# Kernel tuning notes

Measured on AMD Instinct MI355X. Metric: run time of the kernel, lower is better.

Reference implementation:

```python
import jax, jax.numpy as jnp
import numpy as np
from jax import lax

B, C, H, W = 32, 256, 56, 56
NH, LC, DIL = 8, 7, 8  # heads, window size, dilation; H == LC*DIL -> exact dilated partition
N = LC * LC
DH = C // NH
SCALE = DH ** (-0.5)


def _rel_index():
    ch = np.arange(LC)
    coords = np.stack(np.meshgrid(ch, ch, indexing='ij')).reshape(2, -1)  # (2, 49)
    rel = (coords[:, :, None] - coords[:, None, :]).transpose(1, 2, 0)  # (49,49,2)
    rel[..., 0] += LC - 1
    rel[..., 1] += LC - 1
    rel[..., 0] *= 2 * LC - 1
    return jnp.asarray(rel.sum(-1))  # (49,49) int

REL_IDX = _rel_index()


def _layernorm(x, w, b, eps=1e-5):
    m = x.mean(-1, keepdims=True)
    v = ((x - m) ** 2).mean(-1, keepdims=True)
    return (x - m) * lax.rsqrt(v + eps) * w + b


def setup_inputs() -> dict:
    key = jax.random.key(0)
    ks = jax.random.split(key, 8)
    def n(k, shape, s=0.02):
        return jax.random.normal(k, shape, jnp.float32) * s
    return {
        'x': jax.random.normal(ks[0], (B, C, H, W), jnp.float32),
        'cpe_w': n(ks[1], (C, 1, 3, 3)),
        'cpe_b': jnp.zeros((C,), jnp.float32),
        'ln1_w': jnp.ones((C,), jnp.float32),
        'ln1_b': jnp.zeros((C,), jnp.float32),
        'rpb': n(ks[2], ((2 * LC - 1) ** 2, NH)),
        'qkv_w': n(ks[3], (C, 3 * C)),
        'qkv_b': jnp.zeros((3 * C,), jnp.float32),
        'proj_w': n(ks[4], (C, C)),
        'proj_b': jnp.zeros((C,), jnp.float32),
        'ln2_w': jnp.ones((C,), jnp.float32),
        'ln2_b': jnp.zeros((C,), jnp.float32),
        'fc1_w': n(ks[5], (C, 4 * C)),
        'fc1_b': jnp.zeros((4 * C,), jnp.float32),
        'fc2_w': n(ks[6], (4 * C, C)),
        'fc2_b': jnp.zeros((C,), jnp.float32),
    }


def reference(x, cpe_w, cpe_b, ln1_w, ln1_b, rpb, qkv_w, qkv_b, proj_w, proj_b,
              ln2_w, ln2_b, fc1_w, fc1_b, fc2_w, fc2_b):
    # CPE: depthwise 3x3 conv, residual
    cpe = lax.conv_general_dilated(x, cpe_w, (1, 1), 'SAME',
                                   dimension_numbers=('NCHW', 'OIHW', 'NCHW'),
                                   feature_group_count=C)
    x = x + cpe + cpe_b[None, :, None, None]
    x = x.transpose(0, 2, 3, 1)  # B,H,W,C
    shortcut = x
    xn = _layernorm(x, ln1_w, ln1_b)
    # dilated window partition (LD!=0): window (i,j) gathers pixels (i+DIL*t, j+DIL*u)
    xw = xn.reshape(B, LC, DIL, LC, DIL, C).transpose(0, 2, 4, 1, 3, 5)  # B,i,j,t,u,C
    x1 = xw.reshape(B * DIL * DIL, N, C)
    # window attention with relative position bias
    qkv = (x1 @ qkv_w + qkv_b).reshape(-1, N, 3, NH, DH).transpose(2, 0, 3, 1, 4)
    q, k, v = qkv[0] * SCALE, qkv[1], qkv[2]  # (Bn,NH,N,DH)
    attn = jnp.einsum('bhnd,bhmd->bhnm', q, k)
    bias = rpb[REL_IDX].transpose(2, 0, 1)  # (NH,N,N)
    attn = jax.nn.softmax(attn + bias[None], axis=-1)
    o = jnp.einsum('bhnm,bhmd->bhnd', attn, v).transpose(0, 2, 1, 3).reshape(-1, N, C)
    o = o @ proj_w + proj_b
    # scatter windows back to spatial positions (exact inverse of the partition)
    o = o.reshape(B, DIL, DIL, LC, LC, C).transpose(0, 3, 1, 4, 2, 5).reshape(B, H, W, C)
    x = shortcut + o
    h = _layernorm(x, ln2_w, ln2_b)
    h = jax.nn.gelu(h @ fc1_w + fc1_b, approximate=False) @ fc2_w + fc2_b
    x = x + h
    return x.transpose(0, 3, 1, 2)  # B,C,H,W
```

## Files before the change

kernel.cpp:

```cpp
#include <hip/hip_runtime.h>
#include <hip/hip_bf16.h>

#define DEVINL __device__ __forceinline__

constexpr int Cc  = 256;
constexpr int Hh  = 56;
constexpr int Ww  = 56;
constexpr int Tn  = 32 * 56 * 56;
constexpr int HW  = Hh * Ww;
constexpr float SCALEF = 0.17677669529663689f;

typedef __attribute__((ext_vector_type(4))) float f32x4;
typedef __attribute__((ext_vector_type(8))) short bf16x8;

DEVINL unsigned short f2bf(float f) {
  __hip_bfloat16 h = __float2bfloat16(f);
  return *reinterpret_cast<unsigned short*>(&h);
}
DEVINL float bf2f(unsigned short u) {
  union { unsigned int i; float f; } v; v.i = (unsigned int)u << 16; return v.f;
}

#define GLOAD_LDS16(gp, lp) \
  __builtin_amdgcn_global_load_lds((const __attribute__((address_space(1))) void*)(gp), \
                                   (__attribute__((address_space(3))) void*)(lp), 16, 0, 0)

__global__ __launch_bounds__(256) void cpe_kernel(const float* __restrict__ x,
    const float* __restrict__ cw, const float* __restrict__ cb,
    unsigned short* __restrict__ out)
{
  __shared__ unsigned short Xs[16 * 581];
  const int tid = threadIdx.x;
  const int bx  = blockIdx.x;
  const int cg  = bx & 15;
  const int t2  = bx >> 4;
  const int hg  = t2 % 7;
  const int b   = t2 / 7;
  const int c0  = cg * 16;
  const int h0  = hg * 8;

  for (int idx = tid; idx < 16 * 580; idx += 256) {
    const int ci  = idx / 580;
    const int rem = idx - ci * 580;
    const int rr  = rem / 58;
    const int wc  = rem - rr * 58;
    const int h2  = h0 - 1 + rr;
    const int w2  = wc - 1;
    float v = 0.f;
    if (h2 >= 0 && h2 < Hh && w2 >= 0 && w2 < Ww)
      v = x[((size_t)(b * Cc + c0 + ci)) * HW + h2 * Ww + w2];
    Xs[ci * 581 + rem] = f2bf(v);
  }
  __syncthreads();

  const int ci = tid & 15;
  const int c  = c0 + ci;
  float wr9[9];
  #pragma unroll
  for (int i = 0; i < 9; ++i) wr9[i] = cw[c * 9 + i];
  const float cbv = cb[c];
  const unsigned short* Xc = Xs + ci * 581;

  #pragma unroll
  for (int it = 0; it < 7; ++it) {
    const int tg   = it * 16 + (tid >> 4);
    const int tok0 = tg * 4;
    const int hr   = tok0 / 56;
    const int w0   = tok0 - hr * 56;
    float r0v[6], r1v[6], r2v[6];
    #pragma unroll
    for (int j = 0; j < 6; ++j) {
      r0v[j] = bf2f(Xc[hr * 58 + w0 + j]);
      r1v[j] = bf2f(Xc[(hr + 1) * 58 + w0 + j]);
      r2v[j] = bf2f(Xc[(hr + 2) * 58 + w0 + j]);
    }
    unsigned short ov[4];
    #pragma unroll
    for (int t = 0; t < 4; ++t) {
      float acc = r1v[t + 1];
      acc += wr9[0] * r0v[t] + wr9[1] * r0v[t + 1] + wr9[2] * r0v[t + 2];
      acc += wr9[3] * r1v[t] + wr9[4] * r1v[t + 1] + wr9[5] * r1v[t + 2];
      acc += wr9[6] * r2v[t] + wr9[7] * r2v[t + 1] + wr9[8] * r2v[t + 2];
      ov[t] = f2bf(acc + cbv);
    }
    const size_t tbase = (size_t)b * HW + (h0 + hr) * Ww + w0;
    #pragma unroll
    for (int t = 0; t < 4; ++t)
      out[(tbase + t) * Cc + c] = ov[t];
  }
}

__global__ __launch_bounds__(256) void stats_bf16(const unsigned short* __restrict__ in,
    float2* __restrict__ st)
{
  const int lane = threadIdx.x & 63;
  const size_t t = (size_t)blockIdx.x * 4 + (threadIdx.x >> 6);
  const ushort4 v = *reinterpret_cast<const ushort4*>(in + t * Cc + lane * 4);
  const float v0 = bf2f(v.x), v1 = bf2f(v.y), v2 = bf2f(v.z), v3 = bf2f(v.w);
  float s  = v0 + v1 + v2 + v3;
  float sq = v0 * v0 + v1 * v1 + v2 * v2 + v3 * v3;
  #pragma unroll
  for (int o = 32; o >= 1; o >>= 1) {
    s  += __shfl_xor(s, o);
    sq += __shfl_xor(sq, o);
  }
  if (lane == 0) {
    const float mean = s * (1.0f / Cc);
    const float var  = sq * (1.0f / Cc) - mean * mean;
    st[t] = make_float2(mean, rsqrtf(var + 1e-5f));
  }
}

__global__ __launch_bounds__(256) void ln_apply_bf16(const unsigned short* __restrict__ inp,
    const float* __restrict__ w, const float* __restrict__ b,
    unsigned short* __restrict__ out)
{
  const int lane = threadIdx.x & 63;
  const size_t t = (size_t)blockIdx.x * 4 + (threadIdx.x >> 6);
  const ushort4 v = *reinterpret_cast<const ushort4*>(inp + t * Cc + lane * 4);
  const float v0 = bf2f(v.x), v1 = bf2f(v.y), v2 = bf2f(v.z), v3 = bf2f(v.w);
  float s  = v0 + v1 + v2 + v3;
  float sq = v0 * v0 + v1 * v1 + v2 * v2 + v3 * v3;
  #pragma unroll
  for (int o = 32; o >= 1; o >>= 1) {
    s  += __shfl_xor(s, o);
    sq += __shfl_xor(sq, o);
  }
  const float mean = s * (1.0f / Cc);
  const float var  = sq * (1.0f / Cc) - mean * mean;
  const float r    = rsqrtf(var + 1e-5f);
  const float4 w4 = *reinterpret_cast<const float4*>(w + lane * 4);
  const float4 b4 = *reinterpret_cast<const float4*>(b + lane * 4);
  ushort4 o;
  o.x = f2bf((v0 - mean) * r * w4.x + b4.x);
  o.y = f2bf((v1 - mean) * r * w4.y + b4.y);
  o.z = f2bf((v2 - mean) * r * w4.z + b4.z);
  o.w = f2bf((v3 - mean) * r * w4.w + b4.w);
  *reinterpret_cast<ushort4*>(out + t * Cc + lane * 4) = o;
}

template<int QS>
__global__ __launch_bounds__(256) void wconv_kernel(const float* __restrict__ W,
    const float* __restrict__ g, unsigned short* __restrict__ Wt, int K, int N)
{
  __shared__ float Xs[32][33];
  const int kb = blockIdx.x * 32, nb = blockIdx.y * 32;
  const int tn = threadIdx.x & 31, tk = threadIdx.x >> 5;
  #pragma unroll
  for (int i = 0; i < 4; ++i) {
    const int k = kb + tk + i * 8;
    const float gv = g ? g[k] : 1.0f;
    Xs[tk + i * 8][tn] = W[(size_t)k * N + nb + tn] * gv;
  }
  __syncthreads();
  const int wk = threadIdx.x & 31, wn = threadIdx.x >> 5;
  #pragma unroll
  for (int i = 0; i < 4; ++i) {
    const int n = nb + wn + i * 8;
    const float s = (QS && n < 256) ? SCALEF : 1.0f;
    Wt[(size_t)n * K + kb + wk] = f2bf(Xs[wk][wn + i * 8] * s);
  }
}

template<int S>
__global__ __launch_bounds__(256) void colsum_kernel(const float* __restrict__ W,
    const float* __restrict__ g, const float* __restrict__ bvec,
    const float* __restrict__ bias, float* __restrict__ C1, float* __restrict__ CB,
    int K, int N)
{
  __shared__ float red[2][256];
  const int col = blockIdx.x * 64 + (threadIdx.x & 63);
  const int ks  = threadIdx.x >> 6;
  const int kq  = K >> 2;
  float a1 = 0.f, a2 = 0.f;
  for (int k = ks * kq; k < (ks + 1) * kq; ++k) {
    const float wv = W[(size_t)k * N + col];
    a1 += g[k] * wv;
    a2 += bvec[k] * wv;
  }
  red[0][threadIdx.x] = a1;
  red[1][threadIdx.x] = a2;
  __syncthreads();
  if (threadIdx.x < 64) {
    float s1 = 0.f, s2 = 0.f;
    #pragma unroll
    for (int i = 0; i < 4; ++i) { s1 += red[0][threadIdx.x + i * 64]; s2 += red[1][threadIdx.x + i * 64]; }
    const float sc = (S && col < 256) ? SCALEF : 1.0f;
    C1[col] = sc * s1;
    CB[col] = sc * (s2 + bias[col]);
  }
}

__global__ __launch_bounds__(256) void biasgen_kernel(const float* __restrict__ rpb,
    float* __restrict__ biasT)
{
  const int i = blockIdx.x * 256 + threadIdx.x;
  const int h = i >> 12, n = (i >> 6) & 63, m = i & 63;
  float v;
  if (m >= 49) {
    v = -1e30f;
  } else {
    const int nc = n < 49 ? n : 48;
    const int dI = nc / 7 - m / 7 + 6;
    const int dJ = nc % 7 - m % 7 + 6;
    v = rpb[(dI * 13 + dJ) * 8 + h];
  }
  biasT[i] = v;
}

template<int EPI, int OSW>
__global__ __launch_bounds__(256) void mfma_gemm(
    const unsigned short* __restrict__ A, const unsigned short* __restrict__ Bt,
    const float* __restrict__ bias, const float* __restrict__ C1,
    const float2* __restrict__ stats, const unsigned short* __restrict__ resp,
    void* __restrict__ outp, int K, int N, int row0, int n_outer, int n_inner)
{
  __shared__ unsigned short Asm[128 * 64];
  __shared__ unsigned short Bsm[128 * 64];
  const int tid  = threadIdx.x;
  const int lane = tid & 63;
  const int wid  = tid >> 6;
  const int wr   = wid >> 1;
  const int wc   = wid & 1;

  int outer, inner;
  if ((n_outer & 7) == 0) {
    const int slot = blockIdx.x >> 3;
    outer = (slot / n_inner) * 8 + (blockIdx.x & 7);
    inner = slot - (slot / n_inner) * n_inner;
  } else {
    outer = blockIdx.x / n_inner;
    inner = blockIdx.x - outer * n_inner;
  }
  const int bm = (OSW ? inner : outer) * 128;
  const int bn = (OSW ? outer : inner) * 128;

  f32x4 acc[4][4] = {};

  const int srow = (lane >> 3);
  const int skc  = ((lane & 7) ^ srow) * 8;

  for (int k0 = 0; k0 < K; k0 += 64) {
    #pragma unroll
    for (int i = 0; i < 4; ++i) {
      const int ch  = wid * 4 + i;
      const int row = ch * 8 + srow;
      GLOAD_LDS16(A  + (size_t)(bm + row) * K + k0 + skc, &Asm[ch * 512]);
      GLOAD_LDS16(Bt + (size_t)(bn + row) * K + k0 + skc, &Bsm[ch * 512]);
    }
    __syncthreads();

    const int xr = lane & 7;
    const int lg = lane >> 4;
    #pragma unroll
    for (int k32 = 0; k32 < 2; ++k32) {
      const int koff = ((k32 * 4 + lg) ^ xr) * 8;
      bf16x8 af[4], bv[4];
      #pragma unroll
      for (int f = 0; f < 4; ++f) {
        af[f] = *reinterpret_cast<const bf16x8*>(
            &Asm[(wr * 64 + f * 16 + (lane & 15)) * 64 + koff]);
        bv[f] = *reinterpret_cast<const bf16x8*>(
            &Bsm[(wc * 64 + f * 16 + (lane & 15)) * 64 + koff]);
      }
      #pragma unroll
      for (int fm = 0; fm < 4; ++fm)
        #pragma unroll
        for (int fn = 0; fn < 4; ++fn)
          acc[fm][fn] = __builtin_amdgcn_mfma_f32_16x16x32_bf16(
              af[fm], bv[fn], acc[fm][fn], 0, 0, 0);
    }
    __syncthreads();
  }

  const int lr4 = (lane >> 4) * 4;
  const int lc  = lane & 15;
  if constexpr (EPI == 0) {
    float rsv[4][4], rmv[4][4];
    #pragma unroll
    for (int fm = 0; fm < 4; ++fm)
      #pragma unroll
      for (int r = 0; r < 4; ++r) {
        const float2 st = stats[bm + wr * 64 + fm * 16 + lr4 + r];
        rsv[fm][r] = st.y;
        rmv[fm][r] = -st.y * st.x;
      }
    #pragma unroll
    for (int fn = 0; fn < 4; ++fn) {
      const int gcol = bn + wc * 64 + fn * 16 + lc;
      const float c1 = C1[gcol], cb = bias[gcol];
      #pragma unroll
      for (int fm = 0; fm < 4; ++fm)
        #pragma unroll
        for (int r = 0; r < 4; ++r) {
          const int grow = bm + wr * 64 + fm * 16 + lr4 + r;
          const float v = rsv[fm][r] * acc[fm][fn][r] + rmv[fm][r] * c1 + cb;
          ((unsigned short*)outp)[(size_t)grow * N + gcol] = f2bf(v);
        }
    }
  } else if constexpr (EPI == 4) {
    float bch[4][4];
    #pragma unroll
    for (int fm = 0; fm < 4; ++fm)
      #pragma unroll
      for (int r = 0; r < 4; ++r)
        bch[fm][r] = bias[bm + wr * 64 + fm * 16 + lr4 + r];
    #pragma unroll
    for (int fn = 0; fn < 4; ++fn) {
      const int gtok = bn + wc * 64 + fn * 16 + lc;
      const int mg = row0 + gtok;
      const int b  = mg / HW;
      const int sp = mg - b * HW;
      float* ob = (float*)outp + (size_t)b * 256 * HW + sp;
      #pragma unroll
      for (int fm = 0; fm < 4; ++fm)
        #pragma unroll
        for (int r = 0; r < 4; ++r) {
          const int ch = bm + wr * 64 + fm * 16 + lr4 + r;
          float v = acc[fm][fn][r] + bch[fm][r];
          v += bf2f(resp[(size_t)gtok * 256 + ch]);
          ob[(size_t)ch * HW] = v;
        }
    }
  } else {
    #pragma unroll
    for (int fn = 0; fn < 4; ++fn) {
      const int gcol = bn + wc * 64 + fn * 16 + lc;
      const float bvs = bias[gcol];
      #pragma unroll
      for (int fm = 0; fm < 4; ++fm) {
        #pragma unroll
        for (int r = 0; r < 4; ++r) {
          const int grow = bm + wr * 64 + fm * 16 + lr4 + r;
          float v = acc[fm][fn][r] + bvs;
          if constexpr (EPI == 1) {
            v += bf2f(resp[(size_t)grow * 256 + gcol]);
            ((unsigned short*)outp)[(size_t)grow * N + gcol] = f2bf(v);
          } else {
            const float z = 1.5957691f * (v + 0.044715f * v * v * v);
            v = v / (1.0f + __expf(-z));
            ((unsigned short*)outp)[(size_t)grow * N + gcol] = f2bf(v);
          }
        }
      }
    }
  }
}

__global__ __launch_bounds__(256) void attn_mfma(const unsigned short* __restrict__ qkv,
    const float* __restrict__ biasT, unsigned short* __restrict__ outD)
{
  __shared__ char smem[4 * 14848];
  const int tid  = threadIdx.x;
  const int lane = tid & 63;
  const int wid  = tid >> 6;
  char* base = smem + wid * 14848;
  char* Qs = base;
  char* Ks = base + 5120;
  char* Vt = base + 10240;
  char* Ps = base;

  const int blk = blockIdx.x;
  const int b   = blk >> 6;
  const int di  = (blk >> 3) & 7;
  const int dj  = blk & 7;
  const size_t t00 = (size_t)b * HW + di * Ww + dj;

  const int lg = lane >> 4;
  const int lc = lane & 15;

  for (int rep = 0; rep < 2; ++rep) {
    const int h = wid * 2 + rep;

    for (int i = lane; i < 300; i += 64) {
      if (i < 150) reinterpret_cast<unsigned long long*>(Qs + 49 * 80)[i] = 0ull;
      else         reinterpret_cast<unsigned long long*>(Ks + 49 * 80)[i - 150] = 0ull;
    }
    for (int i = lane; i < 192; i += 64) {
      const int row = i / 6, q = i - (i / 6) * 6;
      *reinterpret_cast<unsigned long long*>(Vt + row * 144 + 96 + q * 8) = 0ull;
    }

    for (int idx = lane; idx < 392; idx += 64) {
      const int row = idx >> 3, dq = idx & 7;
      const int li = row / 7, lj = row - (row / 7) * 7;
      const size_t t = t00 + (size_t)(li * 8) * Ww + lj * 8;
      const unsigned short* src = qkv + t * 768 + h * 32 + dq * 4;
      *reinterpret_cast<uint2*>(Qs + row * 80 + dq * 8) =
          *reinterpret_cast<const uint2*>(src);
      *reinterpret_cast<uint2*>(Ks + row * 80 + dq * 8) =
          *reinterpret_cast<const uint2*>(src + 256);
    }
    for (int idx = lane; idx < 784; idx += 64) {
      const int row = idx >> 4, q = idx & 15;
      const int li = row / 7, lj = row - (row / 7) * 7;
      const size_t t = t00 + (size_t)(li * 8) * Ww + lj * 8;
      const unsigned int v = *reinterpret_cast<const unsigned int*>(
          qkv + t * 768 + h * 32 + 512 + q * 2);
      *reinterpret_cast<unsigned short*>(Vt + (2 * q) * 144 + row * 2) =
          (unsigned short)(v & 0xffff);
      *reinterpret_cast<unsigned short*>(Vt + (2 * q + 1) * 144 + row * 2) =
          (unsigned short)(v >> 16);
    }

    f32x4 sacc[4][4] = {};
    {
      bf16x8 af[4], bv[4];
      #pragma unroll
      for (int f = 0; f < 4; ++f) {
        af[f] = *reinterpret_cast<const bf16x8*>(Qs + (f * 16 + lc) * 80 + lg * 16);
        bv[f] = *reinterpret_cast<const bf16x8*>(Ks + (f * 16 + lc) * 80 + lg * 16);
      }
      #pragma unroll
      for (int fm = 0; fm < 4; ++fm)
        #pragma unroll
        for (int fn = 0; fn < 4; ++fn)
          sacc[fm][fn] = __builtin_amdgcn_mfma_f32_16x16x32_bf16(
              af[fm], bv[fn], sacc[fm][fn], 0, 0, 0);
    }

    const float* bh = biasT + h * 4096;
    #pragma unroll
    for (int fm = 0; fm < 4; ++fm) {
      float rowv[4][4];
      #pragma unroll
      for (int r = 0; r < 4; ++r) {
        const int n = fm * 16 + lg * 4 + r;
        #pragma unroll
        for (int fn = 0; fn < 4; ++fn)
          rowv[r][fn] = sacc[fm][fn][r] + bh[n * 64 + fn * 16 + lc];
      }
      #pragma unroll
      for (int r = 0; r < 4; ++r) {
        float mx = fmaxf(fmaxf(rowv[r][0], rowv[r][1]), fmaxf(rowv[r][2], rowv[r][3]));
        #pragma unroll
        for (int o = 8; o >= 1; o >>= 1) mx = fmaxf(mx, __shfl_xor(mx, o));
        float p[4], sm = 0.f;
        #pragma unroll
        for (int fn = 0; fn < 4; ++fn) { p[fn] = __expf(rowv[r][fn] - mx); sm += p[fn]; }
        #pragma unroll
        for (int o = 8; o >= 1; o >>= 1) sm += __shfl_xor(sm, o);
        const float inv = 1.0f / sm;
        const int n = fm * 16 + lg * 4 + r;
        #pragma unroll
        for (int fn = 0; fn < 4; ++fn)
          *reinterpret_cast<unsigned short*>(Ps + n * 144 + (fn * 16 + lc) * 2) =
              f2bf(p[fn] * inv);
      }
    }

    f32x4 oacc[4][2] = {};
    #pragma unroll
    for (int ks = 0; ks < 2; ++ks) {
      bf16x8 pa[4], vb[2];
      #pragma unroll
      for (int fm = 0; fm < 4; ++fm)
        pa[fm] = *reinterpret_cast<const bf16x8*>(
            Ps + (fm * 16 + lc) * 144 + ks * 64 + lg * 16);
      #pragma unroll
      for (int fn = 0; fn < 2; ++fn)
        vb[fn] = *reinterpret_cast<const bf16x8*>(
            Vt + (fn * 16 + lc) * 144 + ks * 64 + lg * 16);
      #pragma unroll
      for (int fm = 0; fm < 4; ++fm)
        #pragma unroll
        for (int fn = 0; fn < 2; ++fn)
          oacc[fm][fn] = __builtin_amdgcn_mfma_f32_16x16x32_bf16(
              pa[fm], vb[fn], oacc[fm][fn], 0, 0, 0);
    }

    #pragma unroll
    for (int fm = 0; fm < 4; ++fm) {
      #pragma unroll
      for (int r = 0; r < 4; ++r) {
        const int n = fm * 16 + lg * 4 + r;
        if (n < 49) {
          const int li = n / 7, lj = n - (n / 7) * 7;
          const size_t t = t00 + (size_t)(li * 8) * Ww + lj * 8;
          outD[t * 256 + h * 32 + lc]      = f2bf(oacc[fm][0][r]);
          outD[t * 256 + h * 32 + 16 + lc] = f2bf(oacc[fm][1][r]);
        }
      }
    }
  }
}

extern "C" void kernel_launch(void* const* d_in, const int* in_sizes, int n_in,
                              void* d_out, int out_size, void* d_ws, size_t ws_size,
                              hipStream_t stream) {
  (void)in_sizes; (void)n_in; (void)out_size;
  const float* x      = (const float*)d_in[0];
  const float* cpe_w  = (const float*)d_in[1];
  const float* cpe_b  = (const float*)d_in[2];
  const float* ln1_w  = (const float*)d_in[3];
  const float* ln1_b  = (const float*)d_in[4];
  const float* rpb    = (const float*)d_in[5];
  const float* qkv_w  = (const float*)d_in[6];
  const float* qkv_b  = (const float*)d_in[7];
  const float* proj_w = (const float*)d_in[8];
  const float* proj_b = (const float*)d_in[9];
  const float* ln2_w  = (const float*)d_in[10];
  const float* ln2_b  = (const float*)d_in[11];
  const float* fc1_w  = (const float*)d_in[12];
  const float* fc1_b  = (const float*)d_in[13];
  const float* fc2_w  = (const float*)d_in[14];
  const float* fc2_b  = (const float*)d_in[15];

  char* ws = (char*)d_ws;
  unsigned short* qkv_wt  = (unsigned short*)(ws);
  unsigned short* proj_wt = (unsigned short*)(ws + 393216);
  unsigned short* fc1_wt  = (unsigned short*)(ws + 524288);
  unsigned short* fc2_wt  = (unsigned short*)(ws + 1048576);
  float*  C1q = (float*)(ws + 1572864);
  float*  CBq = (float*)(ws + 1575936);

  int NB_rt;
  if      (ws_size >= 311000000ull) NB_rt = 32;
  else if (ws_size >= 157000000ull) NB_rt = 16;
  else                              NB_rt = 8;
  const int MCHrt = NB_rt * HW;
  const int NCH   = 32 / NB_rt;
  const int NOUT  = MCHrt / 128;

  unsigned short *slotX, *slotQ, *slotE;
  float2* statsFull = nullptr;
  float*  biasTp;
  if (NB_rt == 8) {
    slotX  = (unsigned short*)(ws + 1579008);
    slotQ  = (unsigned short*)(ws + 14424064);
    slotE  = (unsigned short*)(ws + 65804288);
    biasTp = (float*)(ws + 65804288 + 200704);
  } else {
    biasTp    = (float*)(ws + 1579008);
    statsFull = (float2*)(ws + 1710080);
    size_t o = 2512896;
    slotX = (unsigned short*)(ws + o); o += (size_t)MCHrt * 256 * 2;
    slotQ = (unsigned short*)(ws + o); o += (size_t)MCHrt * 1024 * 2;
    slotE = (unsigned short*)(ws + o);
  }

  unsigned short* Araw = (unsigned short*)d_out + 25690112;

  wconv_kernel<1><<<dim3(8, 24), 256, 0, stream>>>(qkv_w,  ln1_w,  qkv_wt,  256, 768);
  wconv_kernel<0><<<dim3(8, 8),  256, 0, stream>>>(proj_w, nullptr, proj_wt, 256, 256);
  wconv_kernel<0><<<dim3(8, 32), 256, 0, stream>>>(fc1_w,  nullptr, fc1_wt,  256, 1024);
  wconv_kernel<0><<<dim3(32, 8), 256, 0, stream>>>(fc2_w,  nullptr, fc2_wt,  1024, 256);
  colsum_kernel<1><<<12, 256, 0, stream>>>(qkv_w, ln1_w, ln1_b, qkv_b, C1q, CBq, 256, 768);

  cpe_kernel<<<32 * 7 * 16, 256, 0, stream>>>(x, cpe_w, cpe_b, Araw);

  if (NB_rt != 8) {
    stats_bf16<<<Tn / 4, 256, 0, stream>>>(Araw, statsFull);
    biasgen_kernel<<<128, 256, 0, stream>>>(rpb, biasTp);
  }

  for (int c = 0; c < NCH; ++c) {
    const int r0 = c * MCHrt;
    const unsigned short* Ac = Araw + (size_t)r0 * Cc;
    const float2* stp;
    if (NB_rt == 8) {
      float2* stloc = (float2*)slotE;
      stats_bf16<<<MCHrt / 4, 256, 0, stream>>>(Ac, stloc);
      biasgen_kernel<<<128, 256, 0, stream>>>(rpb, biasTp);
      stp = stloc;
    } else {
      stp = statsFull + r0;
    }
    mfma_gemm<0, 0><<<NOUT * 6, 256, 0, stream>>>(
        Ac, qkv_wt, CBq, C1q, stp, nullptr, slotQ, 256, 768, 0, NOUT, 6);
    attn_mfma<<<NB_rt * 64, 256, 0, stream>>>(slotQ, biasTp, slotX);
    mfma_gemm<1, 0><<<NOUT * 2, 256, 0, stream>>>(
        slotX, proj_wt, proj_b, nullptr, nullptr, Ac, slotE, 256, 256, 0, NOUT, 2);
    ln_apply_bf16<<<MCHrt / 4, 256, 0, stream>>>(slotE, ln2_w, ln2_b, slotX);
    mfma_gemm<2, 0><<<NOUT * 8, 256, 0, stream>>>(
        slotX, fc1_wt, fc1_b, nullptr, nullptr, nullptr, slotQ, 256, 1024, 0, NOUT, 8);
    mfma_gemm<4, 1><<<NOUT * 2, 256, 0, stream>>>(
        fc2_wt, slotQ, fc2_b, nullptr, nullptr, slotE, d_out, 1024, 256, r0, NOUT, 2);
  }
}
```

Before: 662.3 us.

## Cap token chunk at 16 images and split MLP into halves for L2 residency

```diff
diff --git a/kernel.cpp b/kernel.cpp
--- a/kernel.cpp
+++ b/kernel.cpp
@@ -223,15 +223,10 @@
   const int wr   = wid >> 1;
   const int wc   = wid & 1;
 
-  int outer, inner;
-  if ((n_outer & 7) == 0) {
-    const int slot = blockIdx.x >> 3;
-    outer = (slot / n_inner) * 8 + (blockIdx.x & 7);
-    inner = slot - (slot / n_inner) * n_inner;
-  } else {
-    outer = blockIdx.x / n_inner;
-    inner = blockIdx.x - outer * n_inner;
-  }
+  const int slot  = blockIdx.x >> 3;
+  const int outer = (slot / n_inner) * 8 + (blockIdx.x & 7);
+  const int inner = slot - (slot / n_inner) * n_inner;
+  if (outer >= n_outer) return;
   const int bm = (OSW ? inner : outer) * 128;
   const int bn = (OSW ? outer : inner) * 128;
 
@@ -514,10 +509,7 @@
   float*  C1q = (float*)(ws + 1572864);
   float*  CBq = (float*)(ws + 1575936);
 
-  int NB_rt;
-  if      (ws_size >= 311000000ull) NB_rt = 32;
-  else if (ws_size >= 157000000ull) NB_rt = 16;
-  else                              NB_rt = 8;
+  const int NB_rt = (ws_size >= 157000000ull) ? 16 : 8;
   const int MCHrt = NB_rt * HW;
   const int NCH   = 32 / NB_rt;
   const int NOUT  = MCHrt / 128;
@@ -535,7 +527,7 @@
     statsFull = (float2*)(ws + 1710080);
     size_t o = 2512896;
     slotX = (unsigned short*)(ws + o); o += (size_t)MCHrt * 256 * 2;
-    slotQ = (unsigned short*)(ws + o); o += (size_t)MCHrt * 1024 * 2;
+    slotQ = (unsigned short*)(ws + o); o += (size_t)MCHrt * 768 * 2;
     slotE = (unsigned short*)(ws + o);
   }
 
@@ -572,9 +564,25 @@
     mfma_gemm<1, 0><<<NOUT * 2, 256, 0, stream>>>(
         slotX, proj_wt, proj_b, nullptr, nullptr, Ac, slotE, 256, 256, 0, NOUT, 2);
     ln_apply_bf16<<<MCHrt / 4, 256, 0, stream>>>(slotE, ln2_w, ln2_b, slotX);
-    mfma_gemm<2, 0><<<NOUT * 8, 256, 0, stream>>>(
-        slotX, fc1_wt, fc1_b, nullptr, nullptr, nullptr, slotQ, 256, 1024, 0, NOUT, 8);
-    mfma_gemm<4, 1><<<NOUT * 2, 256, 0, stream>>>(
-        fc2_wt, slotQ, fc2_b, nullptr, nullptr, slotE, d_out, 1024, 256, r0, NOUT, 2);
-  }
-}
+
+    if (NB_rt == 8) {
+      mfma_gemm<2, 0><<<((NOUT + 7) & ~7) * 8, 256, 0, stream>>>(
+          slotX, fc1_wt, fc1_b, nullptr, nullptr, nullptr, slotQ, 256, 1024, 0, NOUT, 8);
+      mfma_gemm<4, 1><<<((NOUT + 7) & ~7) * 2, 256, 0, stream>>>(
+          fc2_wt, slotQ, fc2_b, nullptr, nullptr, slotE, d_out, 1024, 256, r0, NOUT, 2);
+    } else {
+      const int HTOK = MCHrt / 2;
+      const int NOH  = HTOK / 128;
+      const int NOHP = (NOH + 7) & ~7;
+      for (int half = 0; half < 2; ++half) {
+        const int off = half * HTOK;
+        mfma_gemm<2, 0><<<NOHP * 8, 256, 0, stream>>>(
+            slotX + (size_t)off * 256, fc1_wt, fc1_b, nullptr, nullptr, nullptr,
+            slotQ, 256, 1024, 0, NOH, 8);
+        mfma_gemm<4, 1><<<NOHP * 2, 256, 0, stream>>>(
+            fc2_wt, slotQ, fc2_b, nullptr, nullptr, slotE + (size_t)off * 256,
+            d_out, 1024, 256, r0 + off, NOH, 2);
+      }
+    }
+  }
+}
```

New measurement: 679.9 us. 2.7% more time.

## Fold LN2 into fc1 GEMM epilogue, pad CPE LDS rows, unify block swizzle

Applied to the files above, without the earlier changes.

```diff
diff --git a/kernel.cpp b/kernel.cpp
--- a/kernel.cpp
+++ b/kernel.cpp
@@ -20,6 +20,10 @@
 DEVINL float bf2f(unsigned short u) {
   union { unsigned int i; float f; } v; v.i = (unsigned int)u << 16; return v.f;
 }
+DEVINL float gelu_fast(float v) {
+  const float z = 1.5957691f * (v + 0.044715f * v * v * v);
+  return v / (1.0f + __expf(-z));
+}
 
 #define GLOAD_LDS16(gp, lp) \
   __builtin_amdgcn_global_load_lds((const __attribute__((address_space(1))) void*)(gp), \
@@ -29,7 +33,7 @@
     const float* __restrict__ cw, const float* __restrict__ cb,
     unsigned short* __restrict__ out)
 {
-  __shared__ unsigned short Xs[16 * 581];
+  __shared__ unsigned short Xs[16 * 620];
   const int tid = threadIdx.x;
   const int bx  = blockIdx.x;
   const int cg  = bx & 15;
@@ -49,7 +53,7 @@
     float v = 0.f;
     if (h2 >= 0 && h2 < Hh && w2 >= 0 && w2 < Ww)
       v = x[((size_t)(b * Cc + c0 + ci)) * HW + h2 * Ww + w2];
-    Xs[ci * 581 + rem] = f2bf(v);
+    Xs[ci * 620 + rr * 60 + wc] = f2bf(v);
   }
   __syncthreads();
 
@@ -59,7 +63,7 @@
   #pragma unroll
   for (int i = 0; i < 9; ++i) wr9[i] = cw[c * 9 + i];
   const float cbv = cb[c];
-  const unsigned short* Xc = Xs + ci * 581;
+  const unsigned short* Xc = Xs + ci * 620;
 
   #pragma unroll
   for (int it = 0; it < 7; ++it) {
@@ -67,20 +71,21 @@
     const int tok0 = tg * 4;
     const int hr   = tok0 / 56;
     const int w0   = tok0 - hr * 56;
-    float r0v[6], r1v[6], r2v[6];
-    #pragma unroll
-    for (int j = 0; j < 6; ++j) {
-      r0v[j] = bf2f(Xc[hr * 58 + w0 + j]);
-      r1v[j] = bf2f(Xc[(hr + 1) * 58 + w0 + j]);
-      r2v[j] = bf2f(Xc[(hr + 2) * 58 + w0 + j]);
+    float rv[3][6];
+    #pragma unroll
+    for (int j = 0; j < 3; ++j) {
+      const ushort4 a = *reinterpret_cast<const ushort4*>(Xc + (hr + j) * 60 + w0);
+      const ushort2 e = *reinterpret_cast<const ushort2*>(Xc + (hr + j) * 60 + w0 + 4);
+      rv[j][0] = bf2f(a.x); rv[j][1] = bf2f(a.y); rv[j][2] = bf2f(a.z);
+      rv[j][3] = bf2f(a.w); rv[j][4] = bf2f(e.x); rv[j][5] = bf2f(e.y);
     }
     unsigned short ov[4];
     #pragma unroll
     for (int t = 0; t < 4; ++t) {
-      float acc = r1v[t + 1];
-      acc += wr9[0] * r0v[t] + wr9[1] * r0v[t + 1] + wr9[2] * r0v[t + 2];
-      acc += wr9[3] * r1v[t] + wr9[4] * r1v[t + 1] + wr9[5] * r1v[t + 2];
-      acc += wr9[6] * r2v[t] + wr9[7] * r2v[t + 1] + wr9[8] * r2v[t + 2];
+      float acc = rv[1][t + 1];
+      acc += wr9[0] * rv[0][t] + wr9[1] * rv[0][t + 1] + wr9[2] * rv[0][t + 2];
+      acc += wr9[3] * rv[1][t] + wr9[4] * rv[1][t + 1] + wr9[5] * rv[1][t + 2];
+      acc += wr9[6] * rv[2][t] + wr9[7] * rv[2][t + 1] + wr9[8] * rv[2][t + 2];
       ov[t] = f2bf(acc + cbv);
     }
     const size_t tbase = (size_t)b * HW + (h0 + hr) * Ww + w0;
@@ -111,34 +116,6 @@
   }
 }
 
-__global__ __launch_bounds__(256) void ln_apply_bf16(const unsigned short* __restrict__ inp,
-    const float* __restrict__ w, const float* __restrict__ b,
-    unsigned short* __restrict__ out)
-{
-  const int lane = threadIdx.x & 63;
-  const size_t t = (size_t)blockIdx.x * 4 + (threadIdx.x >> 6);
-  const ushort4 v = *reinterpret_cast<const ushort4*>(inp + t * Cc + lane * 4);
-  const float v0 = bf2f(v.x), v1 = bf2f(v.y), v2 = bf2f(v.z), v3 = bf2f(v.w);
-  float s  = v0 + v1 + v2 + v3;
-  float sq = v0 * v0 + v1 * v1 + v2 * v2 + v3 * v3;
-  #pragma unroll
-  for (int o = 32; o >= 1; o >>= 1) {
-    s  += __shfl_xor(s, o);
-    sq += __shfl_xor(sq, o);
-  }
-  const float mean = s * (1.0f / Cc);
-  const float var  = sq * (1.0f / Cc) - mean * mean;
-  const float r    = rsqrtf(var + 1e-5f);
-  const float4 w4 = *reinterpret_cast<const float4*>(w + lane * 4);
-  const float4 b4 = *reinterpret_cast<const float4*>(b + lane * 4);
-  ushort4 o;
-  o.x = f2bf((v0 - mean) * r * w4.x + b4.x);
-  o.y = f2bf((v1 - mean) * r * w4.y + b4.y);
-  o.z = f2bf((v2 - mean) * r * w4.z + b4.z);
-  o.w = f2bf((v3 - mean) * r * w4.w + b4.w);
-  *reinterpret_cast<ushort4*>(out + t * Cc + lane * 4) = o;
-}
-
 template<int QS>
 __global__ __launch_bounds__(256) void wconv_kernel(const float* __restrict__ W,
     const float* __restrict__ g, unsigned short* __restrict__ Wt, int K, int N)
@@ -223,15 +200,10 @@
   const int wr   = wid >> 1;
   const int wc   = wid & 1;
 
-  int outer, inner;
-  if ((n_outer & 7) == 0) {
-    const int slot = blockIdx.x >> 3;
-    outer = (slot / n_inner) * 8 + (blockIdx.x & 7);
-    inner = slot - (slot / n_inner) * n_inner;
-  } else {
-    outer = blockIdx.x / n_inner;
-    inner = blockIdx.x - outer * n_inner;
-  }
+  const int slot  = blockIdx.x >> 3;
+  const int outer = (slot / n_inner) * 8 + (blockIdx.x & 7);
+  const int inner = slot - (slot / n_inner) * n_inner;
+  if (outer >= n_outer) return;
   const int bm = (OSW ? inner : outer) * 128;
   const int bn = (OSW ? outer : inner) * 128;
 
@@ -275,7 +247,7 @@
 
   const int lr4 = (lane >> 4) * 4;
   const int lc  = lane & 15;
-  if constexpr (EPI == 0) {
+  if constexpr (EPI == 0 || EPI == 5) {
     float rsv[4][4], rmv[4][4];
     #pragma unroll
     for (int fm = 0; fm < 4; ++fm)
@@ -294,7 +266,8 @@
         #pragma unroll
         for (int r = 0; r < 4; ++r) {
           const int grow = bm + wr * 64 + fm * 16 + lr4 + r;
-          const float v = rsv[fm][r] * acc[fm][fn][r] + rmv[fm][r] * c1 + cb;
+          float v = rsv[fm][r] * acc[fm][fn][r] + rmv[fm][r] * c1 + cb;
+          if constexpr (EPI == 5) v = gelu_fast(v);
           ((unsigned short*)outp)[(size_t)grow * N + gcol] = f2bf(v);
         }
     }
@@ -333,14 +306,8 @@
         for (int r = 0; r < 4; ++r) {
           const int grow = bm + wr * 64 + fm * 16 + lr4 + r;
           float v = acc[fm][fn][r] + bvs;
-          if constexpr (EPI == 1) {
-            v += bf2f(resp[(size_t)grow * 256 + gcol]);
-            ((unsigned short*)outp)[(size_t)grow * N + gcol] = f2bf(v);
-          } else {
-            const float z = 1.5957691f * (v + 0.044715f * v * v * v);
-            v = v / (1.0f + __expf(-z));
-            ((unsigned short*)outp)[(size_t)grow * N + gcol] = f2bf(v);
-          }
+          v += bf2f(resp[(size_t)grow * 256 + gcol]);
+          ((unsigned short*)outp)[(size_t)grow * N + gcol] = f2bf(v);
         }
       }
     }
@@ -513,27 +480,27 @@
   unsigned short* fc2_wt  = (unsigned short*)(ws + 1048576);
   float*  C1q = (float*)(ws + 1572864);
   float*  CBq = (float*)(ws + 1575936);
-
-  int NB_rt;
-  if      (ws_size >= 311000000ull) NB_rt = 32;
-  else if (ws_size >= 157000000ull) NB_rt = 16;
-  else                              NB_rt = 8;
+  float*  C1f = (float*)(ws + 1579008);
+  float*  CBf = (float*)(ws + 1583104);
+
+  const int NB_rt = (ws_size >= 311000000ull) ? 32 : 8;
   const int MCHrt = NB_rt * HW;
   const int NCH   = 32 / NB_rt;
   const int NOUT  = MCHrt / 128;
+  const int NOUTP = (NOUT + 7) & ~7;
 
   unsigned short *slotX, *slotQ, *slotE;
-  float2* statsFull = nullptr;
+  float2* stats1Full = nullptr;
   float*  biasTp;
   if (NB_rt == 8) {
-    slotX  = (unsigned short*)(ws + 1579008);
-    slotQ  = (unsigned short*)(ws + 14424064);
-    slotE  = (unsigned short*)(ws + 65804288);
-    biasTp = (float*)(ws + 65804288 + 200704);
+    slotX  = (unsigned short*)(ws + 1587200);
+    slotQ  = (unsigned short*)(ws + 1587200 + 12845056);
+    slotE  = (unsigned short*)(ws + 1587200 + 12845056 + 51380224);
+    biasTp = (float*)((char*)slotE + 200704);
   } else {
-    biasTp    = (float*)(ws + 1579008);
-    statsFull = (float2*)(ws + 1710080);
-    size_t o = 2512896;
+    biasTp     = (float*)(ws + 1587200);
+    stats1Full = (float2*)(ws + 1718272);
+    size_t o = 2521088;
     slotX = (unsigned short*)(ws + o); o += (size_t)MCHrt * 256 * 2;
     slotQ = (unsigned short*)(ws + o); o += (size_t)MCHrt * 1024 * 2;
     slotE = (unsigned short*)(ws + o);
@@ -543,38 +510,40 @@
 
   wconv_kernel<1><<<dim3(8, 24), 256, 0, stream>>>(qkv_w,  ln1_w,  qkv_wt,  256, 768);
   wconv_kernel<0><<<dim3(8, 8),  256, 0, stream>>>(proj_w, nullptr, proj_wt, 256, 256);
-  wconv_kernel<0><<<dim3(8, 32), 256, 0, stream>>>(fc1_w,  nullptr, fc1_wt,  256, 1024);
+  wconv_kernel<0><<<dim3(8, 32), 256, 0, stream>>>(fc1_w,  ln2_w,  fc1_wt,  256, 1024);
   wconv_kernel<0><<<dim3(32, 8), 256, 0, stream>>>(fc2_w,  nullptr, fc2_wt,  1024, 256);
   colsum_kernel<1><<<12, 256, 0, stream>>>(qkv_w, ln1_w, ln1_b, qkv_b, C1q, CBq, 256, 768);
+  colsum_kernel<0><<<16, 256, 0, stream>>>(fc1_w, ln2_w, ln2_b, fc1_b, C1f, CBf, 256, 1024);
 
   cpe_kernel<<<32 * 7 * 16, 256, 0, stream>>>(x, cpe_w, cpe_b, Araw);
 
   if (NB_rt != 8) {
-    stats_bf16<<<Tn / 4, 256, 0, stream>>>(Araw, statsFull);
+    stats_bf16<<<Tn / 4, 256, 0, stream>>>(Araw, stats1Full);
     biasgen_kernel<<<128, 256, 0, stream>>>(rpb, biasTp);
   }
 
   for (int c = 0; c < NCH; ++c) {
     const int r0 = c * MCHrt;
     const unsigned short* Ac = Araw + (size_t)r0 * Cc;
-    const float2* stp;
+    const float2* stp1;
     if (NB_rt == 8) {
       float2* stloc = (float2*)slotE;
       stats_bf16<<<MCHrt / 4, 256, 0, stream>>>(Ac, stloc);
       biasgen_kernel<<<128, 256, 0, stream>>>(rpb, biasTp);
-      stp = stloc;
+      stp1 = stloc;
     } else {
-      stp = statsFull + r0;
-    }
-    mfma_gemm<0, 0><<<NOUT * 6, 256, 0, stream>>>(
-        Ac, qkv_wt, CBq, C1q, stp, nullptr, slotQ, 256, 768, 0, NOUT, 6);
+      stp1 = stats1Full + r0;
+    }
+    mfma_gemm<0, 0><<<NOUTP * 6, 256, 0, stream>>>(
+        Ac, qkv_wt, CBq, C1q, stp1, nullptr, slotQ, 256, 768, 0, NOUT, 6);
     attn_mfma<<<NB_rt * 64, 256, 0, stream>>>(slotQ, biasTp, slotX);
-    mfma_gemm<1, 0><<<NOUT * 2, 256, 0, stream>>>(
+    mfma_gemm<1, 0><<<NOUTP * 2, 256, 0, stream>>>(
         slotX, proj_wt, proj_b, nullptr, nullptr, Ac, slotE, 256, 256, 0, NOUT, 2);
-    ln_apply_bf16<<<MCHrt / 4, 256, 0, stream>>>(slotE, ln2_w, ln2_b, slotX);
-    mfma_gemm<2, 0><<<NOUT * 8, 256, 0, stream>>>(
-        slotX, fc1_wt, fc1_b, nullptr, nullptr, nullptr, slotQ, 256, 1024, 0, NOUT, 8);
-    mfma_gemm<4, 1><<<NOUT * 2, 256, 0, stream>>>(
+    float2* stats2 = (float2*)slotX;
+    stats_bf16<<<MCHrt / 4, 256, 0, stream>>>(slotE, stats2);
+    mfma_gemm<5, 0><<<NOUTP * 8, 256, 0, stream>>>(
+        slotE, fc1_wt, CBf, C1f, stats2, nullptr, slotQ, 256, 1024, 0, NOUT, 8);
+    mfma_gemm<4, 1><<<NOUTP * 2, 256, 0, stream>>>(
         fc2_wt, slotQ, fc2_b, nullptr, nullptr, slotE, d_out, 1024, 256, r0, NOUT, 2);
   }
 }
```

After: 673.1 us. About the same (+1.6%).
